# Kernel optimization log

Hardware: AMD Instinct MI355X
Metric: run time of the kernel (lower is better)

## Reference

```python
import jax, jax.numpy as jnp
import numpy as np

NEG_SLOPE = 0.2


def gat_conv(x, edge_index, W, a_src, a_dst, b, concat):
    """PyG-style GATConv: add self-loops, linear, edge attention, scatter-softmax, scatter-add."""
    N = x.shape[0]
    H, C = a_src.shape
    loop = jnp.arange(N)
    src = jnp.concatenate([edge_index[0], loop])  # source j (messages flow j -> i)
    dst = jnp.concatenate([edge_index[1], loop])  # target i (aggregation node)
    h = (x @ W).reshape(N, H, C)                  # [N,H,C]
    alpha_s = jnp.sum(h * a_src, axis=-1)         # [N,H]
    alpha_d = jnp.sum(h * a_dst, axis=-1)         # [N,H]
    e = jax.nn.leaky_relu(alpha_s[src] + alpha_d[dst], NEG_SLOPE)  # [E,H]
    # numerically stable scatter-softmax over edges grouped by destination node
    m = jax.ops.segment_max(e, dst, num_segments=N)                # [N,H]
    ex = jnp.exp(e - m[dst])
    denom = jax.ops.segment_sum(ex, dst, num_segments=N)           # [N,H]
    alpha = ex / (denom[dst] + 1e-16)                              # [E,H]
    out = jax.ops.segment_sum(h[src] * alpha[:, :, None], dst, num_segments=N)  # [N,H,C]
    out = out.reshape(N, H * C) if concat else out.mean(axis=1)
    return out + b


def setup_inputs() -> dict:
    key = jax.random.key(0)
    ks = jax.random.split(key, 12)
    N, E, F_IN, HID, OUT, HEADS = 100000, 1600000, 128, 128, 64, 4
    C1 = HID // HEADS
    x = jax.random.normal(ks[0], (N, F_IN), dtype=jnp.float32)
    edge_index = jax.random.randint(ks[1], (2, E), 0, N, dtype=jnp.int64)
    s = 0.05
    return {
        "x": x,
        "edge_index": edge_index,
        "W1": jax.random.normal(ks[2], (F_IN, HEADS * C1), dtype=jnp.float32) * s,
        "a_src1": jax.random.normal(ks[3], (HEADS, C1), dtype=jnp.float32) * s,
        "a_dst1": jax.random.normal(ks[4], (HEADS, C1), dtype=jnp.float32) * s,
        "b1": jnp.zeros((HEADS * C1,), dtype=jnp.float32),
        "W2": jax.random.normal(ks[5], (HID, OUT), dtype=jnp.float32) * s,
        "a_src2": jax.random.normal(ks[6], (1, OUT), dtype=jnp.float32) * s,
        "a_dst2": jax.random.normal(ks[7], (1, OUT), dtype=jnp.float32) * s,
        "b2": jnp.zeros((OUT,), dtype=jnp.float32),
    }


def reference(x, edge_index, W1, a_src1, a_dst1, b1, W2, a_src2, a_dst2, b2):
    h = jax.nn.elu(gat_conv(x, edge_index, W1, a_src1, a_dst1, b1, concat=True))
    # F.dropout(p=0.5, training=False) is the identity in eval mode
    out = gat_conv(h, edge_index, W2, a_src2, a_dst2, b2, concat=False)
    return out
```

## Files before the change

### kernel.cpp

```cpp
#include <hip/hip_runtime.h>
#include <hip/hip_fp16.h>
#include <math.h>
#include <string.h>


#define BSH 9
#define DPB 512
#define NBK 256
#define CH1 16384
#define DBINS 512
#define OCH 1024
#define HB 128
#define LOG2E 1.44269504088896f

using half8 = __attribute__((ext_vector_type(8))) _Float16;
using floatx4 = __attribute__((ext_vector_type(4))) float;

__device__ __forceinline__ float exp2_fast(float x) {
#if __has_builtin(__builtin_amdgcn_exp2f)
    return __builtin_amdgcn_exp2f(x);
#else
    return exp2f(x);
#endif
}

__device__ __forceinline__ void wfrag(const float* __restrict__ W, __half* __restrict__ WtF,
                                      int NC, int fid) {
    int col = fid & 15, quad = (fid >> 4) & 3, rest = fid >> 6;
    int NT = NC >> 4;
    int t = rest & (NT - 1), k0s = rest / NT;
    int n = t * 16 + col;
    int k = k0s * 32 + quad * 8;
#pragma unroll
    for (int j = 0; j < 8; ++j)
        WtF[fid * 8 + j] = __float2half(W[(k + j) * NC + n]);
}


__global__ __launch_bounds__(256) void bucket_hist(const int* __restrict__ ei, int E, int N,
                                                   unsigned* __restrict__ bcount,
                                                   const float* __restrict__ W1,
                                                   const float* __restrict__ W2,
                                                   __half* __restrict__ WtF1,
                                                   __half* __restrict__ WtF2) {
    if (blockIdx.x >= HB) {
        int tid = (blockIdx.x - HB) * 256 + threadIdx.x;
        if (tid < 2048) wfrag(W1, WtF1, 128, tid);
        else if (tid < 3072) wfrag(W2, WtF2, 64, tid - 2048);
        return;
    }
    __shared__ unsigned hist[NBK];
    int t = threadIdx.x;
    hist[t] = 0;
    __syncthreads();
    int Etot = E + N;
    for (int k = blockIdx.x * 256 + t; k < Etot; k += HB * 256) {
        int d = (k < E) ? ei[E + k] : (k - E);
        atomicAdd(&hist[d >> BSH], 1u);
    }
    __syncthreads();
    unsigned c = hist[t];
    if (c) atomicAdd(&bcount[t], c);
}

__global__ void scan_buckets(const unsigned* __restrict__ bcount, unsigned* __restrict__ bbase,
                             unsigned* __restrict__ bcursor) {
    __shared__ unsigned s[NBK];
    int t = threadIdx.x;
    unsigned v = bcount[t];
    s[t] = v;
    __syncthreads();
    for (int o = 1; o < NBK; o <<= 1) {
        unsigned add = (t >= o) ? s[t - o] : 0;
        __syncthreads();
        s[t] += add;
        __syncthreads();
    }
    unsigned excl = s[t] - v;
    bbase[t] = excl;
    bcursor[t] = excl;
    if (t == NBK - 1) bbase[NBK] = excl + v;
}

__global__ __launch_bounds__(256) void bucket_scatter(const int* __restrict__ ei, int E, int N,
                                                      unsigned* __restrict__ bcursor,
                                                      unsigned* __restrict__ rec) {
    __shared__ unsigned hist[NBK];
    __shared__ unsigned base[NBK];
    int t = threadIdx.x;
    hist[t] = 0;
    __syncthreads();
    int Etot = E + N;
    int k0 = blockIdx.x * CH1;
    int k1 = min(k0 + CH1, Etot);
    for (int k = k0 + t; k < k1; k += 256) {
        int d = (k < E) ? ei[E + k] : (k - E);
        atomicAdd(&hist[d >> BSH], 1u);
    }
    __syncthreads();
    unsigned c = hist[t];
    base[t] = c ? atomicAdd(&bcursor[t], c) : 0u;
    hist[t] = 0;
    __syncthreads();
    for (int k = k0 + t; k < k1; k += 256) {
        int s, d;
        if (k < E) { s = ei[k]; d = ei[E + k]; } else { s = d = k - E; }
        int b = d >> BSH;
        unsigned r = atomicAdd(&hist[b], 1u);
        rec[base[b] + r] = (unsigned)s | ((unsigned)(d & (DPB - 1)) << 17);
    }
}

__global__ __launch_bounds__(256) void bucket_sort(const unsigned* __restrict__ rec,
                                                   const unsigned* __restrict__ bbase,
                                                   int* __restrict__ offs, int* __restrict__ srcs,
                                                   unsigned* __restrict__ deghist,
                                                   int N, int Etot) {
    __shared__ unsigned hist[DPB];
    __shared__ unsigned tsum[256];
    __shared__ unsigned deg_l[DBINS];
    int t = threadIdx.x, bb = blockIdx.x;
    unsigned r0 = bbase[bb], r1 = bbase[bb + 1];
    hist[t] = 0;
    hist[t + 256] = 0;
    deg_l[t] = 0;
    deg_l[t + 256] = 0;
    __syncthreads();
    int dlo = bb << BSH;
    for (unsigned k = r0 + t; k < r1; k += 256) {
        unsigned e = rec[k];
        atomicAdd(&hist[e >> 17], 1u);
    }
    __syncthreads();
    unsigned h0 = hist[2 * t], h1 = hist[2 * t + 1];
    int d0 = dlo + 2 * t;
    if (d0 < N) atomicAdd(&deg_l[min(h0, (unsigned)(DBINS - 1))], 1u);
    if (d0 + 1 < N) atomicAdd(&deg_l[min(h1, (unsigned)(DBINS - 1))], 1u);
    tsum[t] = h0 + h1;
    __syncthreads();
    for (int o = 1; o < 256; o <<= 1) {
        unsigned a = (t >= o) ? tsum[t - o] : 0;
        __syncthreads();
        tsum[t] += a;
        __syncthreads();
    }
    unsigned tb = tsum[t] - (h0 + h1);
    if (d0 < N) offs[d0] = (int)(r0 + tb);
    if (d0 + 1 < N) offs[d0 + 1] = (int)(r0 + tb + h0);
    hist[2 * t] = tb;
    hist[2 * t + 1] = tb + h0;
    __syncthreads();
    for (unsigned k = r0 + t; k < r1; k += 256) {
        unsigned e = rec[k];
        unsigned r = atomicAdd(&hist[e >> 17], 1u);
        srcs[r0 + r] = (int)(e & 0x1FFFFu);
    }
    if (bb == 0 && t == 0) offs[N] = Etot;
    unsigned c0 = deg_l[t], c1 = deg_l[t + 256];
    if (c0) atomicAdd(&deghist[t], c0);
    if (c1) atomicAdd(&deghist[t + 256], c1);
}


__global__ void scan_deg(const unsigned* __restrict__ deghist, unsigned* __restrict__ degcur) {
    __shared__ unsigned s[DBINS];
    int t = threadIdx.x;
    unsigned v = deghist[t];
    s[t] = v;
    __syncthreads();
    for (int o = 1; o < DBINS; o <<= 1) {
        unsigned a = (t >= o) ? s[t - o] : 0;
        __syncthreads();
        s[t] += a;
        __syncthreads();
    }
    degcur[t] = s[t] - v;
}

__global__ __launch_bounds__(256) void order_scatter(const int* __restrict__ offs,
                                                     unsigned* __restrict__ degcur,
                                                     int* __restrict__ order, int N) {
    __shared__ unsigned hist[DBINS];
    __shared__ unsigned base[DBINS];
    int t = threadIdx.x;
    hist[t] = 0;
    hist[t + 256] = 0;
    __syncthreads();
    int k0 = blockIdx.x * OCH, k1 = min(k0 + OCH, N);
    for (int k = k0 + t; k < k1; k += 256) {
        int deg = offs[k + 1] - offs[k];
        atomicAdd(&hist[min(deg, DBINS - 1)], 1u);
    }
    __syncthreads();
    for (int i = t; i < DBINS; i += 256) {
        unsigned c = hist[i];
        base[i] = c ? atomicAdd(&degcur[i], c) : 0u;
        hist[i] = 0;
    }
    __syncthreads();
    for (int k = k0 + t; k < k1; k += 256) {
        int deg = offs[k + 1] - offs[k];
        int b = min(deg, DBINS - 1);
        unsigned r = atomicAdd(&hist[b], 1u);
        order[base[b] + r] = k;
    }
}


template <int NC, int H, typename InT>
__global__ __launch_bounds__(256) void gemm_mfma(const InT* __restrict__ A,
                                                 const __half* __restrict__ WtF,
                                                 __half* __restrict__ C,
                                                 const float* __restrict__ a_src,
                                                 const float* __restrict__ a_dst,
                                                 float* __restrict__ as,
                                                 float* __restrict__ ad, int M) {
    constexpr int NT = NC / 16;
    constexpr int TPH = NT / H;
    int wave = threadIdx.x >> 6;
    int lane = threadIdx.x & 63;
    int quad = lane >> 4, col = lane & 15;
    int row0 = blockIdx.x * 64 + wave * 16;
    int arow = row0 + col;
    if (arow >= M) arow = M - 1;
    floatx4 acc[NT] = {};
    const half8* wf = reinterpret_cast<const half8*>(WtF) + lane;
#pragma unroll
    for (int k0s = 0; k0s < 4; ++k0s) {
        int k0 = k0s * 32;
        half8 af;
        if constexpr (sizeof(InT) == 4) {
            const float* ap = (const float*)A + (size_t)arow * 128 + k0 + quad * 8;
            float4 v0 = *reinterpret_cast<const float4*>(ap);
            float4 v1 = *reinterpret_cast<const float4*>(ap + 4);
            af[0] = (_Float16)v0.x; af[1] = (_Float16)v0.y;
            af[2] = (_Float16)v0.z; af[3] = (_Float16)v0.w;
            af[4] = (_Float16)v1.x; af[5] = (_Float16)v1.y;
            af[6] = (_Float16)v1.z; af[7] = (_Float16)v1.w;
        } else {
            af = *reinterpret_cast<const half8*>((const __half*)A + (size_t)arow * 128 + k0 + quad * 8);
        }
#pragma unroll
        for (int t = 0; t < NT; ++t) {
            half8 bf = wf[(k0s * NT + t) * 64];
            acc[t] = __builtin_amdgcn_mfma_f32_16x16x32_f16(af, bf, acc[t], 0, 0, 0);
        }
    }
    float sa[NT], da[NT];
#pragma unroll
    for (int t = 0; t < NT; ++t) {
        sa[t] = a_src[t * 16 + col];
        da[t] = a_dst[t * 16 + col];
    }
    int rbase = row0 + quad * 4;
#pragma unroll
    for (int reg = 0; reg < 4; ++reg) {
        int row = rbase + reg;
        bool live = row < M;
        if (live) {
#pragma unroll
            for (int t = 0; t < NT; ++t)
                C[(size_t)row * NC + t * 16 + col] = __float2half(acc[t][reg]);
        }
#pragma unroll
        for (int h = 0; h < H; ++h) {
            float ps = 0.f, pd = 0.f;
#pragma unroll
            for (int tt = 0; tt < TPH; ++tt) {
                int t = h * TPH + tt;
                ps = fmaf(acc[t][reg], sa[t], ps);
                pd = fmaf(acc[t][reg], da[t], pd);
            }
#pragma unroll
            for (int o = 1; o < 16; o <<= 1) {
                ps += __shfl_xor(ps, o, 64);
                pd += __shfl_xor(pd, o, 64);
            }
            if (col == 0 && live) {
                as[(size_t)row * H + h] = ps * LOG2E;
                ad[(size_t)row * H + h] = pd * LOG2E;
            }
        }
    }
}


template <int H, int ROWS, int CW, bool DOELU, typename OutT>
__global__ __launch_bounds__(256) void aggregateQ(const __half* __restrict__ h,
                                                  const float* __restrict__ as,
                                                  const float* __restrict__ ad,
                                                  const int* __restrict__ offs,
                                                  const int* __restrict__ srcs,
                                                  const int* __restrict__ order,
                                                  const float* __restrict__ bias,
                                                  OutT* __restrict__ out, int N) {
    constexpr int CPL = CW / 16;
    constexpr int NH2 = CPL / 2;
    unsigned wave = (blockIdx.x * blockDim.x + threadIdx.x) >> 6;
    unsigned lane = threadIdx.x & 63;
    unsigned lig = lane & 15;
    unsigned idx = wave * 4u + (lane >> 4);
    bool live = idx < (unsigned)N;
    unsigned nc = (unsigned)order[live ? ((unsigned)N - 1u - idx) : 0u];
    unsigned chan = lig * CPL;
    unsigned head = (chan * H) / ROWS;
    float adv = ad[nc * H + head];
    int e0 = offs[nc], e1 = offs[nc + 1];
    int deg = e1 - e0, e1m1 = e1 - 1;
    int md = deg;
    md = max(md, __shfl_xor(md, 16, 64));
    md = max(md, __shfl_xor(md, 32, 64));
    float2 acc[NH2] = {};
    float den = 0.f;
    for (int k = 0; k < md; k += 2) {
        unsigned ja = (unsigned)srcs[min(e0 + k, e1m1)];
        unsigned jb = (unsigned)srcs[min(e0 + k + 1, e1m1)];
        float ta = as[ja * H + head] + adv;
        float tb = as[jb * H + head] + adv;
        __half2 ha[NH2], hb[NH2];
        if constexpr (NH2 == 4) {
            uint4 va = *reinterpret_cast<const uint4*>(h + ja * (unsigned)ROWS + chan);
            uint4 vb = *reinterpret_cast<const uint4*>(h + jb * (unsigned)ROWS + chan);
            memcpy(ha, &va, 16);
            memcpy(hb, &vb, 16);
        } else {
            uint2 va = *reinterpret_cast<const uint2*>(h + ja * (unsigned)ROWS + chan);
            uint2 vb = *reinterpret_cast<const uint2*>(h + jb * (unsigned)ROWS + chan);
            memcpy(ha, &va, 8);
            memcpy(hb, &vb, 8);
        }
        float xa = exp2_fast(fmaxf(ta, 0.2f * ta));
        float xb = exp2_fast(fmaxf(tb, 0.2f * tb));
        xa = (k < deg) ? xa : 0.f;
        xb = (k + 1 < deg) ? xb : 0.f;
#pragma unroll
        for (int q = 0; q < NH2; ++q) {
            float2 fa = __half22float2(ha[q]);
            float2 fb = __half22float2(hb[q]);
            acc[q].x = fmaf(xa, fa.x, acc[q].x);
            acc[q].y = fmaf(xa, fa.y, acc[q].y);
            acc[q].x = fmaf(xb, fb.x, acc[q].x);
            acc[q].y = fmaf(xb, fb.y, acc[q].y);
        }
        den += xa + xb;
    }
    float r = 1.0f / (den + 1e-16f);
    if (!live) return;
    const float* bp = bias + chan;
    if constexpr (sizeof(OutT) == 2) {
        __half2 st[NH2];
#pragma unroll
        for (int q = 0; q < NH2; ++q) {
            float v0 = acc[q].x * r + bp[2 * q];
            float v1 = acc[q].y * r + bp[2 * q + 1];
            if constexpr (DOELU) {
                v0 = (v0 > 0.f) ? v0 : expm1f(v0);
                v1 = (v1 > 0.f) ? v1 : expm1f(v1);
            }
            st[q] = __floats2half2_rn(v0, v1);
        }
        if constexpr (NH2 == 4) {
            uint4 v; memcpy(&v, st, 16);
            *reinterpret_cast<uint4*>((__half*)out + nc * (unsigned)ROWS + chan) = v;
        } else {
            uint2 v; memcpy(&v, st, 8);
            *reinterpret_cast<uint2*>((__half*)out + nc * (unsigned)ROWS + chan) = v;
        }
    } else {
        float vs[CPL];
#pragma unroll
        for (int q = 0; q < NH2; ++q) {
            float v0 = acc[q].x * r + bp[2 * q];
            float v1 = acc[q].y * r + bp[2 * q + 1];
            if constexpr (DOELU) {
                v0 = (v0 > 0.f) ? v0 : expm1f(v0);
                v1 = (v1 > 0.f) ? v1 : expm1f(v1);
            }
            vs[2 * q] = v0;
            vs[2 * q + 1] = v1;
        }
#pragma unroll
        for (int q4 = 0; q4 < CPL; q4 += 4) {
            float4 v = make_float4(vs[q4], vs[q4 + 1], vs[q4 + 2], vs[q4 + 3]);
            *reinterpret_cast<float4*>((float*)out + nc * (unsigned)ROWS + chan + q4) = v;
        }
    }
}


extern "C" void kernel_launch(void* const* d_in, const int* in_sizes, int n_in,
                              void* d_out, int out_size, void* d_ws, size_t ws_size,
                              hipStream_t stream) {
    const float* x      = (const float*)d_in[0];
    const int*   ei     = (const int*)d_in[1];
    const float* W1     = (const float*)d_in[2];
    const float* a_src1 = (const float*)d_in[3];
    const float* a_dst1 = (const float*)d_in[4];
    const float* b1     = (const float*)d_in[5];
    const float* W2     = (const float*)d_in[6];
    const float* a_src2 = (const float*)d_in[7];
    const float* a_dst2 = (const float*)d_in[8];
    const float* b2     = (const float*)d_in[9];
    float* out = (float*)d_out;

    const int N = out_size / 64;
    const int E = in_sizes[1] / 2;
    const int Etot = E + N;

    size_t off = 0;
    auto carve = [&](size_t bytes) -> void* {
        void* p = (char*)d_ws + off;
        off += (bytes + 255) & ~(size_t)255;
        return p;
    };
    __half* h1      = (__half*)carve((size_t)N * 128 * 2);
    __half* hmid    = (__half*)carve((size_t)N * 128 * 2);
    float* as1      = (float*)carve((size_t)N * 4 * 4);
    float* ad1      = (float*)carve((size_t)N * 4 * 4);
    float* as2      = (float*)carve((size_t)N * 4);
    float* ad2      = (float*)carve((size_t)N * 4);
    int*   offs     = (int*)carve((size_t)(N + 1) * 4);
    int*   srcs     = (int*)carve((size_t)Etot * 4);
    unsigned* rec   = (unsigned*)carve((size_t)Etot * 4);
    unsigned* ctrs  = (unsigned*)carve((NBK + DBINS) * 4);
    unsigned* bbase   = (unsigned*)carve((NBK + 1) * 4);
    unsigned* bcursor = (unsigned*)carve(NBK * 4);
    unsigned* degcur  = (unsigned*)carve(DBINS * 4);
    __half* WtF1    = (__half*)carve(128 * 128 * 2);
    __half* WtF2    = (__half*)carve(64 * 128 * 2);
    unsigned* bcount  = ctrs;
    unsigned* deghist = ctrs + NBK;
    int* order      = (int*)rec;
    __half* h2      = h1;

    hipMemsetAsync(ctrs, 0, (NBK + DBINS) * sizeof(unsigned), stream);
    bucket_hist<<<HB + 12, 256, 0, stream>>>(ei, E, N, bcount, W1, W2, WtF1, WtF2);
    scan_buckets<<<1, 256, 0, stream>>>(bcount, bbase, bcursor);
    bucket_scatter<<<(Etot + CH1 - 1) / CH1, 256, 0, stream>>>(ei, E, N, bcursor, rec);
    bucket_sort<<<(N + DPB - 1) / DPB, 256, 0, stream>>>(rec, bbase, offs, srcs, deghist, N, Etot);

    scan_deg<<<1, DBINS, 0, stream>>>(deghist, degcur);
    order_scatter<<<(N + OCH - 1) / OCH, 256, 0, stream>>>(offs, degcur, order, N);

    gemm_mfma<128, 4, float><<<(N + 63) / 64, 256, 0, stream>>>(
        x, WtF1, h1, a_src1, a_dst1, as1, ad1, N);
    aggregateQ<4, 128, 128, true, __half><<<(N + 15) / 16, 256, 0, stream>>>(
        h1, as1, ad1, offs, srcs, order, b1, hmid, N);

    gemm_mfma<64, 1, __half><<<(N + 63) / 64, 256, 0, stream>>>(
        hmid, WtF2, h2, a_src2, a_dst2, as2, ad2, N);
    aggregateQ<1, 64, 64, false, float><<<(N + 15) / 16, 256, 0, stream>>>(
        h2, as2, ad2, offs, srcs, order, b2, out, N);
}
```

Measured before the change: 357.4 us.

## Fuse bucket sort, degree scan and layer-1 GEMM; unroll aggregation by four

Merges the per-bucket sort kernel, the degree-histogram scan (done by the last-finishing block via an atomic counter) and the first GEMM into one launch, with block ranges selecting the role, so independent GEMM work runs alongside the sort. This removes two kernel launches and lets the two phases overlap. The aggregation loop now processes four edges per iteration with scalar fp16-to-fp32 accumulators instead of two with half2 pairs, adding memory-level parallelism at some register cost. The last-block scan relies on threadfence and atomic reads for correctness.

```diff
diff --git a/kernel.cpp b/kernel.cpp
--- a/kernel.cpp
+++ b/kernel.cpp
@@ -14,6 +14,7 @@
 #define LOG2E 1.44269504088896f
 
 using half8 = __attribute__((ext_vector_type(8))) _Float16;
+using half4 = __attribute__((ext_vector_type(4))) _Float16;
 using floatx4 = __attribute__((ext_vector_type(4))) float;
 
 __device__ __forceinline__ float exp2_fast(float x) {
@@ -111,116 +112,21 @@
     }
 }
 
-__global__ __launch_bounds__(256) void bucket_sort(const unsigned* __restrict__ rec,
-                                                   const unsigned* __restrict__ bbase,
-                                                   int* __restrict__ offs, int* __restrict__ srcs,
-                                                   unsigned* __restrict__ deghist,
-                                                   int N, int Etot) {
-    __shared__ unsigned hist[DPB];
-    __shared__ unsigned tsum[256];
-    __shared__ unsigned deg_l[DBINS];
-    int t = threadIdx.x, bb = blockIdx.x;
-    unsigned r0 = bbase[bb], r1 = bbase[bb + 1];
-    hist[t] = 0;
-    hist[t + 256] = 0;
-    deg_l[t] = 0;
-    deg_l[t + 256] = 0;
-    __syncthreads();
-    int dlo = bb << BSH;
-    for (unsigned k = r0 + t; k < r1; k += 256) {
-        unsigned e = rec[k];
-        atomicAdd(&hist[e >> 17], 1u);
-    }
-    __syncthreads();
-    unsigned h0 = hist[2 * t], h1 = hist[2 * t + 1];
-    int d0 = dlo + 2 * t;
-    if (d0 < N) atomicAdd(&deg_l[min(h0, (unsigned)(DBINS - 1))], 1u);
-    if (d0 + 1 < N) atomicAdd(&deg_l[min(h1, (unsigned)(DBINS - 1))], 1u);
-    tsum[t] = h0 + h1;
-    __syncthreads();
-    for (int o = 1; o < 256; o <<= 1) {
-        unsigned a = (t >= o) ? tsum[t - o] : 0;
-        __syncthreads();
-        tsum[t] += a;
-        __syncthreads();
-    }
-    unsigned tb = tsum[t] - (h0 + h1);
-    if (d0 < N) offs[d0] = (int)(r0 + tb);
-    if (d0 + 1 < N) offs[d0 + 1] = (int)(r0 + tb + h0);
-    hist[2 * t] = tb;
-    hist[2 * t + 1] = tb + h0;
-    __syncthreads();
-    for (unsigned k = r0 + t; k < r1; k += 256) {
-        unsigned e = rec[k];
-        unsigned r = atomicAdd(&hist[e >> 17], 1u);
-        srcs[r0 + r] = (int)(e & 0x1FFFFu);
-    }
-    if (bb == 0 && t == 0) offs[N] = Etot;
-    unsigned c0 = deg_l[t], c1 = deg_l[t + 256];
-    if (c0) atomicAdd(&deghist[t], c0);
-    if (c1) atomicAdd(&deghist[t + 256], c1);
-}
-
-
-__global__ void scan_deg(const unsigned* __restrict__ deghist, unsigned* __restrict__ degcur) {
-    __shared__ unsigned s[DBINS];
-    int t = threadIdx.x;
-    unsigned v = deghist[t];
-    s[t] = v;
-    __syncthreads();
-    for (int o = 1; o < DBINS; o <<= 1) {
-        unsigned a = (t >= o) ? s[t - o] : 0;
-        __syncthreads();
-        s[t] += a;
-        __syncthreads();
-    }
-    degcur[t] = s[t] - v;
-}
-
-__global__ __launch_bounds__(256) void order_scatter(const int* __restrict__ offs,
-                                                     unsigned* __restrict__ degcur,
-                                                     int* __restrict__ order, int N) {
-    __shared__ unsigned hist[DBINS];
-    __shared__ unsigned base[DBINS];
-    int t = threadIdx.x;
-    hist[t] = 0;
-    hist[t + 256] = 0;
-    __syncthreads();
-    int k0 = blockIdx.x * OCH, k1 = min(k0 + OCH, N);
-    for (int k = k0 + t; k < k1; k += 256) {
-        int deg = offs[k + 1] - offs[k];
-        atomicAdd(&hist[min(deg, DBINS - 1)], 1u);
-    }
-    __syncthreads();
-    for (int i = t; i < DBINS; i += 256) {
-        unsigned c = hist[i];
-        base[i] = c ? atomicAdd(&degcur[i], c) : 0u;
-        hist[i] = 0;
-    }
-    __syncthreads();
-    for (int k = k0 + t; k < k1; k += 256) {
-        int deg = offs[k + 1] - offs[k];
-        int b = min(deg, DBINS - 1);
-        unsigned r = atomicAdd(&hist[b], 1u);
-        order[base[b] + r] = k;
-    }
-}
-
 
 template <int NC, int H, typename InT>
-__global__ __launch_bounds__(256) void gemm_mfma(const InT* __restrict__ A,
-                                                 const __half* __restrict__ WtF,
-                                                 __half* __restrict__ C,
-                                                 const float* __restrict__ a_src,
-                                                 const float* __restrict__ a_dst,
-                                                 float* __restrict__ as,
-                                                 float* __restrict__ ad, int M) {
+__device__ __forceinline__ void gemm_body(int bid, const InT* __restrict__ A,
+                                          const __half* __restrict__ WtF,
+                                          __half* __restrict__ C,
+                                          const float* __restrict__ a_src,
+                                          const float* __restrict__ a_dst,
+                                          float* __restrict__ as,
+                                          float* __restrict__ ad, int M) {
     constexpr int NT = NC / 16;
     constexpr int TPH = NT / H;
     int wave = threadIdx.x >> 6;
     int lane = threadIdx.x & 63;
     int quad = lane >> 4, col = lane & 15;
-    int row0 = blockIdx.x * 64 + wave * 16;
+    int row0 = bid * 64 + wave * 16;
     int arow = row0 + col;
     if (arow >= M) arow = M - 1;
     floatx4 acc[NT] = {};
@@ -284,6 +190,144 @@
     }
 }
 
+template <int NC, int H, typename InT>
+__global__ __launch_bounds__(256) void gemm_mfma(const InT* __restrict__ A,
+                                                 const __half* __restrict__ WtF,
+                                                 __half* __restrict__ C,
+                                                 const float* __restrict__ a_src,
+                                                 const float* __restrict__ a_dst,
+                                                 float* __restrict__ as,
+                                                 float* __restrict__ ad, int M) {
+    gemm_body<NC, H, InT>(blockIdx.x, A, WtF, C, a_src, a_dst, as, ad, M);
+}
+
+
+__global__ __launch_bounds__(256) void sort_gemm1(const unsigned* __restrict__ rec,
+                                                  const unsigned* __restrict__ bbase,
+                                                  int* __restrict__ offs, int* __restrict__ srcs,
+                                                  unsigned* __restrict__ deghist,
+                                                  unsigned* __restrict__ done,
+                                                  unsigned* __restrict__ degcur,
+                                                  int N, int Etot, int NSB,
+                                                  const float* __restrict__ A,
+                                                  const __half* __restrict__ WtF,
+                                                  __half* __restrict__ C,
+                                                  const float* __restrict__ a_src,
+                                                  const float* __restrict__ a_dst,
+                                                  float* __restrict__ as,
+                                                  float* __restrict__ ad) {
+    if ((int)blockIdx.x >= NSB) {
+        gemm_body<128, 4, float>(blockIdx.x - NSB, A, WtF, C, a_src, a_dst, as, ad, N);
+        return;
+    }
+    __shared__ unsigned hist[DPB];
+    __shared__ unsigned tsum[256];
+    __shared__ unsigned deg_l[DBINS];
+    int t = threadIdx.x, bb = blockIdx.x;
+    unsigned r0 = bbase[bb], r1 = bbase[bb + 1];
+    hist[t] = 0;
+    hist[t + 256] = 0;
+    deg_l[t] = 0;
+    deg_l[t + 256] = 0;
+    __syncthreads();
+    int dlo = bb << BSH;
+    for (unsigned k = r0 + t; k < r1; k += 256) {
+        unsigned e = rec[k];
+        atomicAdd(&hist[e >> 17], 1u);
+    }
+    __syncthreads();
+    unsigned h0 = hist[2 * t], h1 = hist[2 * t + 1];
+    int d0 = dlo + 2 * t;
+    if (d0 < N) atomicAdd(&deg_l[min(h0, (unsigned)(DBINS - 1))], 1u);
+    if (d0 + 1 < N) atomicAdd(&deg_l[min(h1, (unsigned)(DBINS - 1))], 1u);
+    tsum[t] = h0 + h1;
+    __syncthreads();
+    for (int o = 1; o < 256; o <<= 1) {
+        unsigned a = (t >= o) ? tsum[t - o] : 0;
+        __syncthreads();
+        tsum[t] += a;
+        __syncthreads();
+    }
+    unsigned tb = tsum[t] - (h0 + h1);
+    if (d0 < N) offs[d0] = (int)(r0 + tb);
+    if (d0 + 1 < N) offs[d0 + 1] = (int)(r0 + tb + h0);
+    hist[2 * t] = tb;
+    hist[2 * t + 1] = tb + h0;
+    __syncthreads();
+    for (unsigned k = r0 + t; k < r1; k += 256) {
+        unsigned e = rec[k];
+        unsigned r = atomicAdd(&hist[e >> 17], 1u);
+        srcs[r0 + r] = (int)(e & 0x1FFFFu);
+    }
+    if (bb == 0 && t == 0) offs[N] = Etot;
+    unsigned c0 = deg_l[t], c1 = deg_l[t + 256];
+    if (c0) atomicAdd(&deghist[t], c0);
+    if (c1) atomicAdd(&deghist[t + 256], c1);
+    __threadfence();
+    __shared__ bool amlast;
+    if (t == 0) amlast = (atomicAdd(done, 1u) == (unsigned)(NSB - 1));
+    __syncthreads();
+    if (!amlast) return;
+    unsigned v0 = atomicAdd(&deghist[t], 0u);
+    unsigned v1 = atomicAdd(&deghist[t + 256], 0u);
+    deg_l[t] = v0;
+    deg_l[t + 256] = v1;
+    __syncthreads();
+    for (int o = 1; o < DBINS; o <<= 1) {
+        unsigned a0 = (t >= o) ? deg_l[t - o] : 0u;
+        unsigned a1 = (t + 256 >= o) ? deg_l[t + 256 - o] : 0u;
+        __syncthreads();
+        deg_l[t] += a0;
+        deg_l[t + 256] += a1;
+        __syncthreads();
+    }
+    degcur[t] = deg_l[t] - v0;
+    degcur[t + 256] = deg_l[t + 256] - v1;
+}
+
+
+__global__ __launch_bounds__(256) void order_scatter(const int* __restrict__ offs,
+                                                     unsigned* __restrict__ degcur,
+                                                     int* __restrict__ order, int N) {
+    __shared__ unsigned hist[DBINS];
+    __shared__ unsigned base[DBINS];
+    int t = threadIdx.x;
+    hist[t] = 0;
+    hist[t + 256] = 0;
+    __syncthreads();
+    int k0 = blockIdx.x * OCH, k1 = min(k0 + OCH, N);
+    for (int k = k0 + t; k < k1; k += 256) {
+        int deg = offs[k + 1] - offs[k];
+        atomicAdd(&hist[min(deg, DBINS - 1)], 1u);
+    }
+    __syncthreads();
+    for (int i = t; i < DBINS; i += 256) {
+        unsigned c = hist[i];
+        base[i] = c ? atomicAdd(&degcur[i], c) : 0u;
+        hist[i] = 0;
+    }
+    __syncthreads();
+    for (int k = k0 + t; k < k1; k += 256) {
+        int deg = offs[k + 1] - offs[k];
+        int b = min(deg, DBINS - 1);
+        unsigned r = atomicAdd(&hist[b], 1u);
+        order[base[b] + r] = k;
+    }
+}
+
+
+template <int CPL>
+__device__ __forceinline__ void ldrow(const __half* __restrict__ p, _Float16* f) {
+    if constexpr (CPL == 8) {
+        half8 v = *reinterpret_cast<const half8*>(p);
+#pragma unroll
+        for (int c = 0; c < 8; ++c) f[c] = v[c];
+    } else {
+        half4 v = *reinterpret_cast<const half4*>(p);
+#pragma unroll
+        for (int c = 0; c < 4; ++c) f[c] = v[c];
+    }
+}
 
 template <int H, int ROWS, int CW, bool DOELU, typename OutT>
 __global__ __launch_bounds__(256) void aggregateQ(const __half* __restrict__ h,
@@ -295,7 +339,6 @@
                                                   const float* __restrict__ bias,
                                                   OutT* __restrict__ out, int N) {
     constexpr int CPL = CW / 16;
-    constexpr int NH2 = CPL / 2;
     unsigned wave = (blockIdx.x * blockDim.x + threadIdx.x) >> 6;
     unsigned lane = threadIdx.x & 63;
     unsigned lig = lane & 15;
@@ -310,56 +353,58 @@
     int md = deg;
     md = max(md, __shfl_xor(md, 16, 64));
     md = max(md, __shfl_xor(md, 32, 64));
-    float2 acc[NH2] = {};
+    float accs[CPL] = {};
     float den = 0.f;
-    for (int k = 0; k < md; k += 2) {
-        unsigned ja = (unsigned)srcs[min(e0 + k, e1m1)];
-        unsigned jb = (unsigned)srcs[min(e0 + k + 1, e1m1)];
-        float ta = as[ja * H + head] + adv;
-        float tb = as[jb * H + head] + adv;
-        __half2 ha[NH2], hb[NH2];
-        if constexpr (NH2 == 4) {
-            uint4 va = *reinterpret_cast<const uint4*>(h + ja * (unsigned)ROWS + chan);
-            uint4 vb = *reinterpret_cast<const uint4*>(h + jb * (unsigned)ROWS + chan);
-            memcpy(ha, &va, 16);
-            memcpy(hb, &vb, 16);
-        } else {
-            uint2 va = *reinterpret_cast<const uint2*>(h + ja * (unsigned)ROWS + chan);
-            uint2 vb = *reinterpret_cast<const uint2*>(h + jb * (unsigned)ROWS + chan);
-            memcpy(ha, &va, 8);
-            memcpy(hb, &vb, 8);
-        }
-        float xa = exp2_fast(fmaxf(ta, 0.2f * ta));
-        float xb = exp2_fast(fmaxf(tb, 0.2f * tb));
-        xa = (k < deg) ? xa : 0.f;
-        xb = (k + 1 < deg) ? xb : 0.f;
-#pragma unroll
-        for (int q = 0; q < NH2; ++q) {
-            float2 fa = __half22float2(ha[q]);
-            float2 fb = __half22float2(hb[q]);
-            acc[q].x = fmaf(xa, fa.x, acc[q].x);
-            acc[q].y = fmaf(xa, fa.y, acc[q].y);
-            acc[q].x = fmaf(xb, fb.x, acc[q].x);
-            acc[q].y = fmaf(xb, fb.y, acc[q].y);
-        }
-        den += xa + xb;
+    for (int k = 0; k < md; k += 4) {
+        int b = e0 + k;
+        unsigned j0 = (unsigned)srcs[min(b, e1m1)];
+        unsigned j1 = (unsigned)srcs[min(b + 1, e1m1)];
+        unsigned j2 = (unsigned)srcs[min(b + 2, e1m1)];
+        unsigned j3 = (unsigned)srcs[min(b + 3, e1m1)];
+        float t0 = as[j0 * H + head] + adv;
+        float t1 = as[j1 * H + head] + adv;
+        float t2 = as[j2 * H + head] + adv;
+        float t3 = as[j3 * H + head] + adv;
+        _Float16 f0[CPL], f1[CPL], f2[CPL], f3[CPL];
+        ldrow<CPL>(h + j0 * (unsigned)ROWS + chan, f0);
+        ldrow<CPL>(h + j1 * (unsigned)ROWS + chan, f1);
+        ldrow<CPL>(h + j2 * (unsigned)ROWS + chan, f2);
+        ldrow<CPL>(h + j3 * (unsigned)ROWS + chan, f3);
+        float x0 = exp2_fast(fmaxf(t0, 0.2f * t0));
+        float x1 = exp2_fast(fmaxf(t1, 0.2f * t1));
+        float x2 = exp2_fast(fmaxf(t2, 0.2f * t2));
+        float x3 = exp2_fast(fmaxf(t3, 0.2f * t3));
+        x0 = (k < deg) ? x0 : 0.f;
+        x1 = (k + 1 < deg) ? x1 : 0.f;
+        x2 = (k + 2 < deg) ? x2 : 0.f;
+        x3 = (k + 3 < deg) ? x3 : 0.f;
+#pragma unroll
+        for (int c = 0; c < CPL; ++c) accs[c] = fmaf(x0, (float)f0[c], accs[c]);
+#pragma unroll
+        for (int c = 0; c < CPL; ++c) accs[c] = fmaf(x1, (float)f1[c], accs[c]);
+#pragma unroll
+        for (int c = 0; c < CPL; ++c) accs[c] = fmaf(x2, (float)f2[c], accs[c]);
+#pragma unroll
+        for (int c = 0; c < CPL; ++c) accs[c] = fmaf(x3, (float)f3[c], accs[c]);
+        den += x0 + x1;
+        den += x2 + x3;
     }
     float r = 1.0f / (den + 1e-16f);
     if (!live) return;
     const float* bp = bias + chan;
+    float vs[CPL];
+#pragma unroll
+    for (int c = 0; c < CPL; ++c) {
+        float v = accs[c] * r + bp[c];
+        if constexpr (DOELU) v = (v > 0.f) ? v : expm1f(v);
+        vs[c] = v;
+    }
     if constexpr (sizeof(OutT) == 2) {
-        __half2 st[NH2];
-#pragma unroll
-        for (int q = 0; q < NH2; ++q) {
-            float v0 = acc[q].x * r + bp[2 * q];
-            float v1 = acc[q].y * r + bp[2 * q + 1];
-            if constexpr (DOELU) {
-                v0 = (v0 > 0.f) ? v0 : expm1f(v0);
-                v1 = (v1 > 0.f) ? v1 : expm1f(v1);
-            }
-            st[q] = __floats2half2_rn(v0, v1);
-        }
-        if constexpr (NH2 == 4) {
+        __half2 st[CPL / 2];
+#pragma unroll
+        for (int q = 0; q < CPL / 2; ++q)
+            st[q] = __floats2half2_rn(vs[2 * q], vs[2 * q + 1]);
+        if constexpr (CPL == 8) {
             uint4 v; memcpy(&v, st, 16);
             *reinterpret_cast<uint4*>((__half*)out + nc * (unsigned)ROWS + chan) = v;
         } else {
@@ -367,18 +412,6 @@
             *reinterpret_cast<uint2*>((__half*)out + nc * (unsigned)ROWS + chan) = v;
         }
     } else {
-        float vs[CPL];
-#pragma unroll
-        for (int q = 0; q < NH2; ++q) {
-            float v0 = acc[q].x * r + bp[2 * q];
-            float v1 = acc[q].y * r + bp[2 * q + 1];
-            if constexpr (DOELU) {
-                v0 = (v0 > 0.f) ? v0 : expm1f(v0);
-                v1 = (v1 > 0.f) ? v1 : expm1f(v1);
-            }
-            vs[2 * q] = v0;
-            vs[2 * q + 1] = v1;
-        }
 #pragma unroll
         for (int q4 = 0; q4 < CPL; q4 += 4) {
             float4 v = make_float4(vs[q4], vs[q4 + 1], vs[q4 + 2], vs[q4 + 3]);
@@ -422,7 +455,7 @@
     int*   offs     = (int*)carve((size_t)(N + 1) * 4);
     int*   srcs     = (int*)carve((size_t)Etot * 4);
     unsigned* rec   = (unsigned*)carve((size_t)Etot * 4);
-    unsigned* ctrs  = (unsigned*)carve((NBK + DBINS) * 4);
+    unsigned* ctrs  = (unsigned*)carve((NBK + DBINS + 8) * 4);
     unsigned* bbase   = (unsigned*)carve((NBK + 1) * 4);
     unsigned* bcursor = (unsigned*)carve(NBK * 4);
     unsigned* degcur  = (unsigned*)carve(DBINS * 4);
@@ -430,24 +463,28 @@
     __half* WtF2    = (__half*)carve(64 * 128 * 2);
     unsigned* bcount  = ctrs;
     unsigned* deghist = ctrs + NBK;
+    unsigned* done    = ctrs + NBK + DBINS;
     int* order      = (int*)rec;
     __half* h2      = h1;
 
-    hipMemsetAsync(ctrs, 0, (NBK + DBINS) * sizeof(unsigned), stream);
+    const int NSB = (N + DPB - 1) / DPB;
+    const int GB  = (N + 63) / 64;
+
+    hipMemsetAsync(ctrs, 0, (NBK + DBINS + 8) * sizeof(unsigned), stream);
     bucket_hist<<<HB + 12, 256, 0, stream>>>(ei, E, N, bcount, W1, W2, WtF1, WtF2);
     scan_buckets<<<1, 256, 0, stream>>>(bcount, bbase, bcursor);
     bucket_scatter<<<(Etot + CH1 - 1) / CH1, 256, 0, stream>>>(ei, E, N, bcursor, rec);
-    bucket_sort<<<(N + DPB - 1) / DPB, 256, 0, stream>>>(rec, bbase, offs, srcs, deghist, N, Etot);
-
-    scan_deg<<<1, DBINS, 0, stream>>>(deghist, degcur);
+
+    sort_gemm1<<<NSB + GB, 256, 0, stream>>>(rec, bbase, offs, srcs, deghist, done, degcur,
+                                             N, Etot, NSB,
+                                             x, WtF1, h1, a_src1, a_dst1, as1, ad1);
+
     order_scatter<<<(N + OCH - 1) / OCH, 256, 0, stream>>>(offs, degcur, order, N);
 
-    gemm_mfma<128, 4, float><<<(N + 63) / 64, 256, 0, stream>>>(
-        x, WtF1, h1, a_src1, a_dst1, as1, ad1, N);
     aggregateQ<4, 128, 128, true, __half><<<(N + 15) / 16, 256, 0, stream>>>(
         h1, as1, ad1, offs, srcs, order, b1, hmid, N);
 
-    gemm_mfma<64, 1, __half><<<(N + 63) / 64, 256, 0, stream>>>(
+    gemm_mfma<64, 1, __half><<<GB, 256, 0, stream>>>(
         hmid, WtF2, h2, a_src2, a_dst2, as2, ad2, N);
     aggregateQ<1, 64, 64, false, float><<<(N + 15) / 16, 256, 0, stream>>>(
         h2, as2, ad2, offs, srcs, order, b2, out, N);
```

Result: no change. 364.5 us (+2.0%).
